# Performance work log

Measured on AMD Instinct MI355X. Metric: run time of the kernel, lower is better.

Reference implementation:

```python
import jax, jax.numpy as jnp
import numpy as np

NUM_EXPERTS = 8
TOP_K = 2
D_HIDDEN = 2048
D_EXPERT = 1024
N_TOKENS = 4096


def setup_inputs() -> dict:
    key = jax.random.key(0)
    ks = jax.random.split(key, 8)
    s_d = 1.0 / np.sqrt(D_HIDDEN).astype(np.float32)
    s_h = 1.0 / np.sqrt(D_EXPERT).astype(np.float32)
    return {
        "x": jax.random.normal(ks[0], (N_TOKENS, D_HIDDEN), jnp.float32),
        "W_g": jax.random.normal(ks[1], (D_HIDDEN, NUM_EXPERTS), jnp.float32) * s_d,
        "W_gate": jax.random.normal(ks[2], (NUM_EXPERTS, D_HIDDEN, D_EXPERT), jnp.float32) * s_d,
        "W_up": jax.random.normal(ks[3], (NUM_EXPERTS, D_HIDDEN, D_EXPERT), jnp.float32) * s_d,
        "W_down": jax.random.normal(ks[4], (NUM_EXPERTS, D_EXPERT, D_HIDDEN), jnp.float32) * s_h,
        "Ws_gate": jax.random.normal(ks[5], (D_HIDDEN, D_EXPERT), jnp.float32) * s_d,
        "Ws_up": jax.random.normal(ks[6], (D_HIDDEN, D_EXPERT), jnp.float32) * s_d,
        "Ws_down": jax.random.normal(ks[7], (D_EXPERT, D_HIDDEN), jnp.float32) * s_h,
    }


def reference(x, W_g, W_gate, W_up, W_down, Ws_gate, Ws_up, Ws_down):
    # Router: softmax logits -> top-k scores/indices (fused_gating_topk)
    probs = jax.nn.softmax(x @ W_g, axis=-1)                      # [N, E]
    scores, idx = jax.lax.top_k(probs, TOP_K)                     # [N, K]
    # Per-(token, expert) combine weight; zero for unrouted experts.
    combine = (jax.nn.one_hot(idx, NUM_EXPERTS, dtype=x.dtype) * scores[..., None]).sum(axis=1)  # [N, E]

    # Routed experts: fused gate/up SiLU with per-token weight scaling, then down-proj.
    gate = jnp.einsum('nd,edh->enh', x, W_gate)                   # [E, N, H]
    up = jnp.einsum('nd,edh->enh', x, W_up)                       # [E, N, H]
    h = jax.nn.silu(gate) * up * combine.T[:, :, None]            # weight=0 kills unrouted tokens
    out = jnp.einsum('enh,ehd->nd', h, W_down)                    # [N, D]

    # Shared expert applied to every token (no routing weight).
    shared = (jax.nn.silu(x @ Ws_gate) * (x @ Ws_up)) @ Ws_down
    return out + shared
```

## Files before the change

### kernel.cpp

```cpp
#include <hip/hip_runtime.h>
#include <cstdint>
#include <cstddef>

#define N_TOK 4096
#define D_HID 2048
#define D_EXP 1024
#define NE 8
#define N_ROUTED (N_TOK * 2)
#define N_ROWS (N_ROUTED + N_TOK)
#define MAX_BLK 112

typedef unsigned short u16;
typedef __bf16 bf16x8 __attribute__((ext_vector_type(8)));
typedef float f32x4 __attribute__((ext_vector_type(4)));

constexpr size_t OFF_XB    = 0;
constexpr size_t OFF_WG    = OFF_XB    + 16777216;
constexpr size_t OFF_WU    = OFF_WG    + 33554432;
constexpr size_t OFF_WD    = OFF_WU    + 33554432;
constexpr size_t OFF_WSG   = OFF_WD    + 33554432;
constexpr size_t OFF_WSU   = OFF_WSG   + 4194304;
constexpr size_t OFF_WSD   = OFF_WSU   + 4194304;
constexpr size_t OFF_H     = OFF_WSD   + 4194304;
constexpr size_t OFF_ROWS  = OFF_H     + 25165824;
constexpr size_t OFF_WSLOT = OFF_ROWS  + 49152;
constexpr size_t OFF_SEG   = OFF_WSLOT + 49152;
constexpr size_t OFF_BLK   = OFF_SEG   + 128;
constexpr size_t OFF_TOPI  = OFF_BLK   + 768;
constexpr size_t OFF_TOPW  = OFF_TOPI  + 32768;

__device__ __forceinline__ u16 f32_to_bf16(float f) {
    union { float f; unsigned int u; } c; c.f = f;
    unsigned int u = c.u;
    return (u16)((u + 0x7FFFu + ((u >> 16) & 1u)) >> 16);
}

__device__ __forceinline__ void gld_lds16(const u16* g, u16* l) {
    __builtin_amdgcn_global_load_lds(
        (const __attribute__((address_space(1))) void*)g,
        (__attribute__((address_space(3))) void*)l,
        16, 0, 0);
}

__global__ void zero_out_kernel(float* __restrict__ out) {
    size_t i = ((size_t)blockIdx.x * 256 + threadIdx.x) * 4;
    float4 z = make_float4(0.f, 0.f, 0.f, 0.f);
    *(float4*)(out + i) = z;
}

__global__ void cvt_x_kernel(const float* __restrict__ x, u16* __restrict__ xb) {
    size_t i = ((size_t)blockIdx.x * 256 + threadIdx.x) * 8;
    float4 a = *(const float4*)(x + i);
    float4 b = *(const float4*)(x + i + 4);
    union { u16 us[8]; uint4 v; } r;
    r.us[0] = f32_to_bf16(a.x); r.us[1] = f32_to_bf16(a.y);
    r.us[2] = f32_to_bf16(a.z); r.us[3] = f32_to_bf16(a.w);
    r.us[4] = f32_to_bf16(b.x); r.us[5] = f32_to_bf16(b.y);
    r.us[6] = f32_to_bf16(b.z); r.us[7] = f32_to_bf16(b.w);
    *(uint4*)(xb + i) = r.v;
}

__global__ void transpose_cvt_kernel(const float* __restrict__ src, u16* __restrict__ dst,
                                     int R, int C) {
    __shared__ float tile[32][33];
    const int tx = threadIdx.x, ty = threadIdx.y;
    const size_t m = (size_t)blockIdx.z * R * C;
    const int c0 = blockIdx.x * 32, r0 = blockIdx.y * 32;
#pragma unroll
    for (int i = 0; i < 4; i++)
        tile[ty + 8 * i][tx] = src[m + (size_t)(r0 + ty + 8 * i) * C + c0 + tx];
    __syncthreads();
#pragma unroll
    for (int i = 0; i < 4; i++)
        dst[m + (size_t)(c0 + ty + 8 * i) * R + r0 + tx] = f32_to_bf16(tile[tx][ty + 8 * i]);
}

__global__ void router_kernel(const float* __restrict__ x, const float* __restrict__ Wg,
                              int* __restrict__ topi, float* __restrict__ topw) {
    const int wave = threadIdx.x >> 6, lane = threadIdx.x & 63;
    const int t = blockIdx.x * 4 + wave;
    const float* xr = x + (size_t)t * D_HID;
    float acc[8] = {0.f, 0.f, 0.f, 0.f, 0.f, 0.f, 0.f, 0.f};
    for (int k = lane; k < D_HID; k += 64) {
        float xv = xr[k];
        float4 w0 = *(const float4*)(Wg + k * 8);
        float4 w1 = *(const float4*)(Wg + k * 8 + 4);
        acc[0] += xv * w0.x; acc[1] += xv * w0.y; acc[2] += xv * w0.z; acc[3] += xv * w0.w;
        acc[4] += xv * w1.x; acc[5] += xv * w1.y; acc[6] += xv * w1.z; acc[7] += xv * w1.w;
    }
#pragma unroll
    for (int e = 0; e < 8; e++)
#pragma unroll
        for (int off = 32; off > 0; off >>= 1)
            acc[e] += __shfl_xor(acc[e], off);
    if (lane == 0) {
        float mx = acc[0];
#pragma unroll
        for (int e = 1; e < 8; e++) mx = fmaxf(mx, acc[e]);
        float p[8], sum = 0.f;
#pragma unroll
        for (int e = 0; e < 8; e++) { p[e] = __expf(acc[e] - mx); sum += p[e]; }
        int i0 = 0; float b0 = p[0];
#pragma unroll
        for (int e = 1; e < 8; e++) if (p[e] > b0) { b0 = p[e]; i0 = e; }
        int i1 = -1; float b1 = -1.f;
#pragma unroll
        for (int e = 0; e < 8; e++) if (e != i0 && p[e] > b1) { b1 = p[e]; i1 = e; }
        float inv = 1.f / sum;
        topi[t * 2] = i0;  topi[t * 2 + 1] = i1;
        topw[t * 2] = b0 * inv; topw[t * 2 + 1] = b1 * inv;
    }
}

__global__ void builder_kernel(const int* __restrict__ topi, const float* __restrict__ topw,
                               int* __restrict__ rows, float* __restrict__ wslot,
                               int* __restrict__ seg, int* __restrict__ blkmap) {
    __shared__ int cnt[8], offs[8];
    const int tid = threadIdx.x;
    if (tid < 8) cnt[tid] = 0;
    __syncthreads();
    for (int i = tid; i < N_TOK * 2; i += 256) atomicAdd(&cnt[topi[i]], 1);
    __syncthreads();
    if (tid == 0) {
        int run = 0;
        for (int e = 0; e < 8; e++) {
            offs[e] = run; seg[e] = run; seg[16 + e] = cnt[e]; run += cnt[e];
        }
        seg[8] = N_ROUTED; seg[16 + 8] = N_TOK;
        int nb = 0;
        for (int e = 0; e < 9; e++) {
            int L = (e < 8) ? cnt[e] : N_TOK;
            for (int rb = 0; rb * 128 < L; rb++) blkmap[nb++] = (e << 8) | rb;
        }
        seg[10] = nb;
    }
    __syncthreads();
    for (int i = tid; i < N_TOK * 2; i += 256) {
        int e = topi[i];
        int p = atomicAdd(&offs[e], 1);
        rows[p] = i >> 1;
        wslot[p] = topw[i];
    }
    for (int t = tid; t < N_TOK; t += 256) {
        rows[N_ROUTED + t] = t;
        wslot[N_ROUTED + t] = 1.0f;
    }
}

__global__ __launch_bounds__(256, 2)
void gemm1_kernel(const u16* __restrict__ xb,
                  const u16* __restrict__ Wg_t, const u16* __restrict__ Wu_t,
                  const u16* __restrict__ Wsg_t, const u16* __restrict__ Wsu_t,
                  const int* __restrict__ rows, const float* __restrict__ wslot,
                  const int* __restrict__ seg, const int* __restrict__ blkmap,
                  u16* __restrict__ h) {
    if ((int)blockIdx.x >= seg[10]) return;
    const int code = blkmap[blockIdx.x];
    const int e = code >> 8, rb = code & 255;
    const int s = seg[e], L = seg[e + 16];
    const u16* Bg = (e < NE) ? Wg_t + (size_t)e * D_EXP * D_HID : Wsg_t;
    const u16* Bu = (e < NE) ? Wu_t + (size_t)e * D_EXP * D_HID : Wsu_t;
    const int cbase = blockIdx.y * 128;

    __shared__ u16 As[128 * 32];
    __shared__ u16 Bgs[128 * 32];
    __shared__ u16 Bus[128 * 32];
    __shared__ int tok_s[128];

    const int tid = threadIdx.x;
    if (tid < 128) {
        int lr = rb * 128 + tid;
        tok_s[tid] = rows[s + (lr < L ? lr : 0)];
    }
    __syncthreads();

    const int lane = tid & 63, wave = tid >> 6;
    const int wm = wave & 1, wn = wave >> 1;
    const int ln = lane & 15, quad = lane >> 4;

    const int lr16 = lane >> 2;
    const int c8 = (lane & 3) * 8;
    const int ra0 = wave * 32 + lr16, ra1 = ra0 + 16;
    const size_t ta0 = (size_t)tok_s[ra0] * D_HID + c8;
    const size_t ta1 = (size_t)tok_s[ra1] * D_HID + c8;
    const u16* pbg0 = Bg + (size_t)(cbase + ra0) * D_HID + c8;
    const u16* pbg1 = Bg + (size_t)(cbase + ra1) * D_HID + c8;
    const u16* pbu0 = Bu + (size_t)(cbase + ra0) * D_HID + c8;
    const u16* pbu1 = Bu + (size_t)(cbase + ra1) * D_HID + c8;
    u16* lA0 = As + (size_t)(wave * 32) * 32;
    u16* lA1 = As + (size_t)(wave * 32 + 16) * 32;
    u16* lG0 = Bgs + (size_t)(wave * 32) * 32;
    u16* lG1 = Bgs + (size_t)(wave * 32 + 16) * 32;
    u16* lU0 = Bus + (size_t)(wave * 32) * 32;
    u16* lU1 = Bus + (size_t)(wave * 32 + 16) * 32;

    f32x4 accg[4][4], accu[4][4];
    const f32x4 zero = {0.f, 0.f, 0.f, 0.f};
#pragma unroll
    for (int i = 0; i < 4; i++)
#pragma unroll
        for (int j = 0; j < 4; j++) { accg[i][j] = zero; accu[i][j] = zero; }

    for (int k0 = 0; k0 < D_HID; k0 += 32) {
        __syncthreads();
        gld_lds16(xb + ta0 + k0, lA0);
        gld_lds16(xb + ta1 + k0, lA1);
        gld_lds16(pbg0 + k0, lG0);
        gld_lds16(pbg1 + k0, lG1);
        gld_lds16(pbu0 + k0, lU0);
        gld_lds16(pbu1 + k0, lU1);
        __syncthreads();
        bf16x8 af[4];
#pragma unroll
        for (int sm = 0; sm < 4; sm++)
            af[sm] = *(const bf16x8*)&As[(wm * 64 + sm * 16 + ln) * 32 + quad * 8];
#pragma unroll
        for (int sn = 0; sn < 4; sn++) {
            const bf16x8 bgf = *(const bf16x8*)&Bgs[(wn * 64 + sn * 16 + ln) * 32 + quad * 8];
            const bf16x8 buf = *(const bf16x8*)&Bus[(wn * 64 + sn * 16 + ln) * 32 + quad * 8];
#pragma unroll
            for (int sm = 0; sm < 4; sm++) {
                accg[sm][sn] = __builtin_amdgcn_mfma_f32_16x16x32_bf16(af[sm], bgf, accg[sm][sn], 0, 0, 0);
                accu[sm][sn] = __builtin_amdgcn_mfma_f32_16x16x32_bf16(af[sm], buf, accu[sm][sn], 0, 0, 0);
            }
        }
    }
#pragma unroll
    for (int sm = 0; sm < 4; sm++) {
#pragma unroll
        for (int r = 0; r < 4; r++) {
            int lrow = rb * 128 + wm * 64 + sm * 16 + quad * 4 + r;
            if (lrow >= L) continue;
            int pos = s + lrow;
            float w = wslot[pos];
#pragma unroll
            for (int sn = 0; sn < 4; sn++) {
                float g = accg[sm][sn][r];
                float u = accu[sm][sn][r];
                float hv = (g / (1.f + __expf(-g))) * u * w;
                int col = cbase + wn * 64 + sn * 16 + ln;
                h[(size_t)pos * D_EXP + col] = f32_to_bf16(hv);
            }
        }
    }
}

__global__ __launch_bounds__(256, 2)
void gemm2_kernel(const u16* __restrict__ h,
                  const u16* __restrict__ Wd_t, const u16* __restrict__ Wsd_t,
                  const int* __restrict__ rows, const int* __restrict__ seg,
                  const int* __restrict__ blkmap, float* __restrict__ out) {
    if ((int)blockIdx.x >= seg[10]) return;
    const int code = blkmap[blockIdx.x];
    const int e = code >> 8, rb = code & 255;
    const int s = seg[e], L = seg[e + 16];
    const u16* B = (e < NE) ? Wd_t + (size_t)e * D_HID * D_EXP : Wsd_t;
    const int cbase = blockIdx.y * 128;

    __shared__ u16 As[128 * 32];
    __shared__ u16 Bs[128 * 32];

    const int tid = threadIdx.x;
    const int lane = tid & 63, wave = tid >> 6;
    const int wm = wave & 1, wn = wave >> 1;
    const int ln = lane & 15, quad = lane >> 4;

    const int lr16 = lane >> 2;
    const int c8 = (lane & 3) * 8;
    const int ra0 = wave * 32 + lr16, ra1 = ra0 + 16;
    const u16* pa0 = h + (size_t)(s + rb * 128 + ra0) * D_EXP + c8;
    const u16* pa1 = h + (size_t)(s + rb * 128 + ra1) * D_EXP + c8;
    const u16* pb0 = B + (size_t)(cbase + ra0) * D_EXP + c8;
    const u16* pb1 = B + (size_t)(cbase + ra1) * D_EXP + c8;
    u16* lA0 = As + (size_t)(wave * 32) * 32;
    u16* lA1 = As + (size_t)(wave * 32 + 16) * 32;
    u16* lB0 = Bs + (size_t)(wave * 32) * 32;
    u16* lB1 = Bs + (size_t)(wave * 32 + 16) * 32;

    f32x4 acc[4][4];
    const f32x4 zero = {0.f, 0.f, 0.f, 0.f};
#pragma unroll
    for (int i = 0; i < 4; i++)
#pragma unroll
        for (int j = 0; j < 4; j++) acc[i][j] = zero;

    for (int k0 = 0; k0 < D_EXP; k0 += 32) {
        __syncthreads();
        gld_lds16(pa0 + k0, lA0);
        gld_lds16(pa1 + k0, lA1);
        gld_lds16(pb0 + k0, lB0);
        gld_lds16(pb1 + k0, lB1);
        __syncthreads();
        bf16x8 af[4];
#pragma unroll
        for (int sm = 0; sm < 4; sm++)
            af[sm] = *(const bf16x8*)&As[(wm * 64 + sm * 16 + ln) * 32 + quad * 8];
#pragma unroll
        for (int sn = 0; sn < 4; sn++) {
            const bf16x8 bfg = *(const bf16x8*)&Bs[(wn * 64 + sn * 16 + ln) * 32 + quad * 8];
#pragma unroll
            for (int sm = 0; sm < 4; sm++)
                acc[sm][sn] = __builtin_amdgcn_mfma_f32_16x16x32_bf16(af[sm], bfg, acc[sm][sn], 0, 0, 0);
        }
    }
#pragma unroll
    for (int sm = 0; sm < 4; sm++) {
#pragma unroll
        for (int r = 0; r < 4; r++) {
            int lrow = rb * 128 + wm * 64 + sm * 16 + quad * 4 + r;
            if (lrow >= L) continue;
            int tok = rows[s + lrow];
#pragma unroll
            for (int sn = 0; sn < 4; sn++) {
                int col = cbase + wn * 64 + sn * 16 + ln;
                atomicAdd(out + (size_t)tok * D_HID + col, acc[sm][sn][r]);
            }
        }
    }
}

extern "C" void kernel_launch(void* const* d_in, const int* in_sizes, int n_in,
                              void* d_out, int out_size, void* d_ws, size_t ws_size,
                              hipStream_t stream) {
    const float* x       = (const float*)d_in[0];
    const float* W_g     = (const float*)d_in[1];
    const float* W_gate  = (const float*)d_in[2];
    const float* W_up    = (const float*)d_in[3];
    const float* W_down  = (const float*)d_in[4];
    const float* Ws_gate = (const float*)d_in[5];
    const float* Ws_up   = (const float*)d_in[6];
    const float* Ws_down = (const float*)d_in[7];
    float* out = (float*)d_out;
    char* ws = (char*)d_ws;

    u16*   xb    = (u16*)(ws + OFF_XB);
    u16*   Wg_t  = (u16*)(ws + OFF_WG);
    u16*   Wu_t  = (u16*)(ws + OFF_WU);
    u16*   Wd_t  = (u16*)(ws + OFF_WD);
    u16*   Wsg_t = (u16*)(ws + OFF_WSG);
    u16*   Wsu_t = (u16*)(ws + OFF_WSU);
    u16*   Wsd_t = (u16*)(ws + OFF_WSD);
    u16*   h     = (u16*)(ws + OFF_H);
    int*   rows  = (int*)(ws + OFF_ROWS);
    float* wslot = (float*)(ws + OFF_WSLOT);
    int*   seg   = (int*)(ws + OFF_SEG);
    int*   blkmap= (int*)(ws + OFF_BLK);
    int*   topi  = (int*)(ws + OFF_TOPI);
    float* topw  = (float*)(ws + OFF_TOPW);

    zero_out_kernel<<<dim3((N_TOK * D_HID) / (256 * 4)), dim3(256), 0, stream>>>(out);
    cvt_x_kernel<<<dim3((N_TOK * D_HID) / (256 * 8)), dim3(256), 0, stream>>>(x, xb);

    dim3 tb(32, 8);
    transpose_cvt_kernel<<<dim3(D_EXP / 32, D_HID / 32, NE), tb, 0, stream>>>(W_gate, Wg_t, D_HID, D_EXP);
    transpose_cvt_kernel<<<dim3(D_EXP / 32, D_HID / 32, NE), tb, 0, stream>>>(W_up, Wu_t, D_HID, D_EXP);
    transpose_cvt_kernel<<<dim3(D_HID / 32, D_EXP / 32, NE), tb, 0, stream>>>(W_down, Wd_t, D_EXP, D_HID);
    transpose_cvt_kernel<<<dim3(D_EXP / 32, D_HID / 32, 1), tb, 0, stream>>>(Ws_gate, Wsg_t, D_HID, D_EXP);
    transpose_cvt_kernel<<<dim3(D_EXP / 32, D_HID / 32, 1), tb, 0, stream>>>(Ws_up, Wsu_t, D_HID, D_EXP);
    transpose_cvt_kernel<<<dim3(D_HID / 32, D_EXP / 32, 1), tb, 0, stream>>>(Ws_down, Wsd_t, D_EXP, D_HID);

    router_kernel<<<dim3(N_TOK / 4), dim3(256), 0, stream>>>(x, W_g, topi, topw);
    builder_kernel<<<dim3(1), dim3(256), 0, stream>>>(topi, topw, rows, wslot, seg, blkmap);

    gemm1_kernel<<<dim3(MAX_BLK, D_EXP / 128), dim3(256), 0, stream>>>(
        xb, Wg_t, Wu_t, Wsg_t, Wsu_t, rows, wslot, seg, blkmap, h);
    gemm2_kernel<<<dim3(MAX_BLK, D_HID / 128), dim3(256), 0, stream>>>(
        h, Wd_t, Wsd_t, rows, seg, blkmap, out);
}
```

Baseline: 623.6 us.

## Replace atomic scatter with bf16 staging plus combine kernel; fuse weight transposes

The down-projection no longer does float atomicAdd scatter into a zeroed output. It writes per-slot bf16 rows into a staging buffer that reuses the gate-weight workspace, and a new combine kernel gathers each token's two routed rows plus its shared row through an inverse slot map. This drops the zero-fill kernel and the atomic traffic. Separately, the six weight transpose/convert launches become two kernels with 64x64 tiles, vectorized float4 loads and 16-byte bf16 stores. The cost is an extra kernel, an extra round-trip through the staging buffer, and bf16 rounding of the partial sums before they are added.

```diff
diff --git a/kernel.cpp b/kernel.cpp
--- a/kernel.cpp
+++ b/kernel.cpp
@@ -28,11 +28,17 @@
 constexpr size_t OFF_BLK   = OFF_SEG   + 128;
 constexpr size_t OFF_TOPI  = OFF_BLK   + 768;
 constexpr size_t OFF_TOPW  = OFF_TOPI  + 32768;
+constexpr size_t OFF_INV   = OFF_TOPW  + 32768;
+constexpr size_t OFF_H2    = OFF_WG;
 
 __device__ __forceinline__ u16 f32_to_bf16(float f) {
     union { float f; unsigned int u; } c; c.f = f;
     unsigned int u = c.u;
     return (u16)((u + 0x7FFFu + ((u >> 16) & 1u)) >> 16);
+}
+__device__ __forceinline__ float bf16_to_f32(u16 v) {
+    union { unsigned int u; float f; } c; c.u = ((unsigned int)v) << 16;
+    return c.f;
 }
 
 __device__ __forceinline__ void gld_lds16(const u16* g, u16* l) {
@@ -40,12 +46,6 @@
         (const __attribute__((address_space(1))) void*)g,
         (__attribute__((address_space(3))) void*)l,
         16, 0, 0);
-}
-
-__global__ void zero_out_kernel(float* __restrict__ out) {
-    size_t i = ((size_t)blockIdx.x * 256 + threadIdx.x) * 4;
-    float4 z = make_float4(0.f, 0.f, 0.f, 0.f);
-    *(float4*)(out + i) = z;
 }
 
 __global__ void cvt_x_kernel(const float* __restrict__ x, u16* __restrict__ xb) {
@@ -60,19 +60,68 @@
     *(uint4*)(xb + i) = r.v;
 }
 
-__global__ void transpose_cvt_kernel(const float* __restrict__ src, u16* __restrict__ dst,
-                                     int R, int C) {
-    __shared__ float tile[32][33];
-    const int tx = threadIdx.x, ty = threadIdx.y;
-    const size_t m = (size_t)blockIdx.z * R * C;
-    const int c0 = blockIdx.x * 32, r0 = blockIdx.y * 32;
-#pragma unroll
-    for (int i = 0; i < 4; i++)
-        tile[ty + 8 * i][tx] = src[m + (size_t)(r0 + ty + 8 * i) * C + c0 + tx];
-    __syncthreads();
-#pragma unroll
-    for (int i = 0; i < 4; i++)
-        dst[m + (size_t)(c0 + ty + 8 * i) * R + r0 + tx] = f32_to_bf16(tile[tx][ty + 8 * i]);
+__global__ void prep_gu_kernel(const float* __restrict__ Wg, const float* __restrict__ Wu,
+                               const float* __restrict__ Wsg, const float* __restrict__ Wsu,
+                               u16* __restrict__ Wg_t, u16* __restrict__ Wu_t,
+                               u16* __restrict__ Wsg_t, u16* __restrict__ Wsu_t) {
+    __shared__ float tile[64][66];
+    const int z = blockIdx.z;
+    const float* src; u16* dst;
+    if (z < 8)        { src = Wg + (size_t)z * (D_HID * D_EXP);       dst = Wg_t + (size_t)z * (D_HID * D_EXP); }
+    else if (z < 16)  { src = Wu + (size_t)(z - 8) * (D_HID * D_EXP); dst = Wu_t + (size_t)(z - 8) * (D_HID * D_EXP); }
+    else if (z == 16) { src = Wsg; dst = Wsg_t; }
+    else              { src = Wsu; dst = Wsu_t; }
+    const int c0 = blockIdx.x * 64, r0 = blockIdx.y * 64;
+    const int tid = threadIdx.x;
+    const int tx = tid & 15, ty = tid >> 4;
+#pragma unroll
+    for (int i = 0; i < 4; i++) {
+        float4 v = *(const float4*)(src + (size_t)(r0 + ty + 16 * i) * D_EXP + c0 + tx * 4);
+        tile[ty + 16 * i][tx * 4 + 0] = v.x;
+        tile[ty + 16 * i][tx * 4 + 1] = v.y;
+        tile[ty + 16 * i][tx * 4 + 2] = v.z;
+        tile[ty + 16 * i][tx * 4 + 3] = v.w;
+    }
+    __syncthreads();
+    const int kx = tid & 7, cy = tid >> 3;
+#pragma unroll
+    for (int j = 0; j < 2; j++) {
+        int n = cy + 32 * j;
+        union { u16 us[8]; uint4 v; } r;
+#pragma unroll
+        for (int m = 0; m < 8; m++) r.us[m] = f32_to_bf16(tile[kx * 8 + m][n]);
+        *(uint4*)(dst + (size_t)(c0 + n) * D_HID + r0 + kx * 8) = r.v;
+    }
+}
+
+__global__ void prep_d_kernel(const float* __restrict__ Wd, const float* __restrict__ Wsd,
+                              u16* __restrict__ Wd_t, u16* __restrict__ Wsd_t) {
+    __shared__ float tile[64][66];
+    const int z = blockIdx.z;
+    const float* src; u16* dst;
+    if (z < 8) { src = Wd + (size_t)z * (D_EXP * D_HID); dst = Wd_t + (size_t)z * (D_EXP * D_HID); }
+    else       { src = Wsd; dst = Wsd_t; }
+    const int c0 = blockIdx.x * 64, r0 = blockIdx.y * 64;
+    const int tid = threadIdx.x;
+    const int tx = tid & 15, ty = tid >> 4;
+#pragma unroll
+    for (int i = 0; i < 4; i++) {
+        float4 v = *(const float4*)(src + (size_t)(r0 + ty + 16 * i) * D_HID + c0 + tx * 4);
+        tile[ty + 16 * i][tx * 4 + 0] = v.x;
+        tile[ty + 16 * i][tx * 4 + 1] = v.y;
+        tile[ty + 16 * i][tx * 4 + 2] = v.z;
+        tile[ty + 16 * i][tx * 4 + 3] = v.w;
+    }
+    __syncthreads();
+    const int kx = tid & 7, cy = tid >> 3;
+#pragma unroll
+    for (int j = 0; j < 2; j++) {
+        int n = cy + 32 * j;
+        union { u16 us[8]; uint4 v; } r;
+#pragma unroll
+        for (int m = 0; m < 8; m++) r.us[m] = f32_to_bf16(tile[kx * 8 + m][n]);
+        *(uint4*)(dst + (size_t)(c0 + n) * D_EXP + r0 + kx * 8) = r.v;
+    }
 }
 
 __global__ void router_kernel(const float* __restrict__ x, const float* __restrict__ Wg,
@@ -114,7 +163,8 @@
 
 __global__ void builder_kernel(const int* __restrict__ topi, const float* __restrict__ topw,
                                int* __restrict__ rows, float* __restrict__ wslot,
-                               int* __restrict__ seg, int* __restrict__ blkmap) {
+                               int* __restrict__ seg, int* __restrict__ blkmap,
+                               int* __restrict__ inv) {
     __shared__ int cnt[8], offs[8];
     const int tid = threadIdx.x;
     if (tid < 8) cnt[tid] = 0;
@@ -140,6 +190,7 @@
         int p = atomicAdd(&offs[e], 1);
         rows[p] = i >> 1;
         wslot[p] = topw[i];
+        inv[i] = p;
     }
     for (int t = tid; t < N_TOK; t += 256) {
         rows[N_ROUTED + t] = t;
@@ -248,8 +299,8 @@
 __global__ __launch_bounds__(256, 2)
 void gemm2_kernel(const u16* __restrict__ h,
                   const u16* __restrict__ Wd_t, const u16* __restrict__ Wsd_t,
-                  const int* __restrict__ rows, const int* __restrict__ seg,
-                  const int* __restrict__ blkmap, float* __restrict__ out) {
+                  const int* __restrict__ seg, const int* __restrict__ blkmap,
+                  u16* __restrict__ h2) {
     if ((int)blockIdx.x >= seg[10]) return;
     const int code = blkmap[blockIdx.x];
     const int e = code >> 8, rb = code & 255;
@@ -309,14 +360,39 @@
         for (int r = 0; r < 4; r++) {
             int lrow = rb * 128 + wm * 64 + sm * 16 + quad * 4 + r;
             if (lrow >= L) continue;
-            int tok = rows[s + lrow];
+            size_t slot = (size_t)(s + lrow);
 #pragma unroll
             for (int sn = 0; sn < 4; sn++) {
                 int col = cbase + wn * 64 + sn * 16 + ln;
-                atomicAdd(out + (size_t)tok * D_HID + col, acc[sm][sn][r]);
+                h2[slot * D_HID + col] = f32_to_bf16(acc[sm][sn][r]);
             }
         }
     }
+}
+
+__global__ void combine_kernel(const u16* __restrict__ h2, const int* __restrict__ inv,
+                               float* __restrict__ out) {
+    const int t = blockIdx.x;
+    const int d = threadIdx.x * 8;
+    const size_t r0 = (size_t)inv[t * 2] * D_HID + d;
+    const size_t r1 = (size_t)inv[t * 2 + 1] * D_HID + d;
+    const size_t r2 = (size_t)(N_ROUTED + t) * D_HID + d;
+    union { uint4 v; u16 us[8]; } a, b, c;
+    a.v = *(const uint4*)(h2 + r0);
+    b.v = *(const uint4*)(h2 + r1);
+    c.v = *(const uint4*)(h2 + r2);
+    float4 lo, hi;
+    lo.x = bf16_to_f32(a.us[0]) + bf16_to_f32(b.us[0]) + bf16_to_f32(c.us[0]);
+    lo.y = bf16_to_f32(a.us[1]) + bf16_to_f32(b.us[1]) + bf16_to_f32(c.us[1]);
+    lo.z = bf16_to_f32(a.us[2]) + bf16_to_f32(b.us[2]) + bf16_to_f32(c.us[2]);
+    lo.w = bf16_to_f32(a.us[3]) + bf16_to_f32(b.us[3]) + bf16_to_f32(c.us[3]);
+    hi.x = bf16_to_f32(a.us[4]) + bf16_to_f32(b.us[4]) + bf16_to_f32(c.us[4]);
+    hi.y = bf16_to_f32(a.us[5]) + bf16_to_f32(b.us[5]) + bf16_to_f32(c.us[5]);
+    hi.z = bf16_to_f32(a.us[6]) + bf16_to_f32(b.us[6]) + bf16_to_f32(c.us[6]);
+    hi.w = bf16_to_f32(a.us[7]) + bf16_to_f32(b.us[7]) + bf16_to_f32(c.us[7]);
+    float* o = out + (size_t)t * D_HID + d;
+    *(float4*)o = lo;
+    *(float4*)(o + 4) = hi;
 }
 
 extern "C" void kernel_launch(void* const* d_in, const int* in_sizes, int n_in,
@@ -341,29 +417,27 @@
     u16*   Wsu_t = (u16*)(ws + OFF_WSU);
     u16*   Wsd_t = (u16*)(ws + OFF_WSD);
     u16*   h     = (u16*)(ws + OFF_H);
+    u16*   h2    = (u16*)(ws + OFF_H2);
     int*   rows  = (int*)(ws + OFF_ROWS);
     float* wslot = (float*)(ws + OFF_WSLOT);
     int*   seg   = (int*)(ws + OFF_SEG);
     int*   blkmap= (int*)(ws + OFF_BLK);
     int*   topi  = (int*)(ws + OFF_TOPI);
     float* topw  = (float*)(ws + OFF_TOPW);
-
-    zero_out_kernel<<<dim3((N_TOK * D_HID) / (256 * 4)), dim3(256), 0, stream>>>(out);
+    int*   inv   = (int*)(ws + OFF_INV);
+
     cvt_x_kernel<<<dim3((N_TOK * D_HID) / (256 * 8)), dim3(256), 0, stream>>>(x, xb);
-
-    dim3 tb(32, 8);
-    transpose_cvt_kernel<<<dim3(D_EXP / 32, D_HID / 32, NE), tb, 0, stream>>>(W_gate, Wg_t, D_HID, D_EXP);
-    transpose_cvt_kernel<<<dim3(D_EXP / 32, D_HID / 32, NE), tb, 0, stream>>>(W_up, Wu_t, D_HID, D_EXP);
-    transpose_cvt_kernel<<<dim3(D_HID / 32, D_EXP / 32, NE), tb, 0, stream>>>(W_down, Wd_t, D_EXP, D_HID);
-    transpose_cvt_kernel<<<dim3(D_EXP / 32, D_HID / 32, 1), tb, 0, stream>>>(Ws_gate, Wsg_t, D_HID, D_EXP);
-    transpose_cvt_kernel<<<dim3(D_EXP / 32, D_HID / 32, 1), tb, 0, stream>>>(Ws_up, Wsu_t, D_HID, D_EXP);
-    transpose_cvt_kernel<<<dim3(D_HID / 32, D_EXP / 32, 1), tb, 0, stream>>>(Ws_down, Wsd_t, D_EXP, D_HID);
+    prep_gu_kernel<<<dim3(D_EXP / 64, D_HID / 64, 18), dim3(256), 0, stream>>>(
+        W_gate, W_up, Ws_gate, Ws_up, Wg_t, Wu_t, Wsg_t, Wsu_t);
+    prep_d_kernel<<<dim3(D_HID / 64, D_EXP / 64, 9), dim3(256), 0, stream>>>(
+        W_down, Ws_down, Wd_t, Wsd_t);
 
     router_kernel<<<dim3(N_TOK / 4), dim3(256), 0, stream>>>(x, W_g, topi, topw);
-    builder_kernel<<<dim3(1), dim3(256), 0, stream>>>(topi, topw, rows, wslot, seg, blkmap);
+    builder_kernel<<<dim3(1), dim3(256), 0, stream>>>(topi, topw, rows, wslot, seg, blkmap, inv);
 
     gemm1_kernel<<<dim3(MAX_BLK, D_EXP / 128), dim3(256), 0, stream>>>(
         xb, Wg_t, Wu_t, Wsg_t, Wsu_t, rows, wslot, seg, blkmap, h);
     gemm2_kernel<<<dim3(MAX_BLK, D_HID / 128), dim3(256), 0, stream>>>(
-        h, Wd_t, Wsd_t, rows, seg, blkmap, out);
-}
+        h, Wd_t, Wsd_t, seg, blkmap, h2);
+    combine_kernel<<<dim3(N_TOK), dim3(256), 0, stream>>>(h2, inv, out);
+}
```

After: 563.0 us. -9.7%, faster.
